# Kernel tuning notes

Measured on AMD Instinct MI355X. Metric: run time of the kernel, lower is better.

The kernel has to match this reference:

```python
import jax, jax.numpy as jnp
import numpy as np

N, E, F, H, L = 10000, 200000, 28, 256, 6
NUM_ATOM, NUM_BOND = 100, 24

def ssp(x):
    # shifted softplus used by SchNet
    return jax.nn.softplus(x) - jnp.log(2.0)

def setup_inputs() -> dict:
    key = jax.random.key(0)
    ks = iter(jax.random.split(key, 64))
    def nrm(shape, scale=0.05):
        return jax.random.normal(next(ks), shape, dtype=jnp.float32) * scale
    inp = {}
    inp['atom_type'] = jax.random.randint(next(ks), (N,), 0, NUM_ATOM)
    inp['r_feat'] = jax.random.normal(next(ks), (N, F), dtype=jnp.float32)
    inp['p_feat'] = jax.random.normal(next(ks), (N, F), dtype=jnp.float32)
    inp['pos'] = jax.random.normal(next(ks), (N, 3), dtype=jnp.float32) * 3.0
    inp['edge_index'] = jax.random.randint(next(ks), (2, E), 0, N)
    inp['edge_type_r'] = jax.random.randint(next(ks), (E,), 0, NUM_BOND)
    inp['edge_type_p'] = jax.random.randint(next(ks), (E,), 0, NUM_BOND)
    # learned parameters
    inp['atom_emb_table'] = nrm((NUM_ATOM, H // 2), 1.0)
    inp['feat_W'] = nrm((F, H // 2))                       # atom_feat_embedding (no bias)
    inp['bond_emb_table'] = nrm((NUM_BOND, H), 1.0)        # edge encoder bond embedding
    inp['edge_mlp_W1'] = nrm((1, H)); inp['edge_mlp_b1'] = jnp.zeros((H,), jnp.float32)
    inp['edge_mlp_W2'] = nrm((H, H)); inp['edge_mlp_b2'] = jnp.zeros((H,), jnp.float32)
    inp['cat_W1'] = nrm((2 * H, H)); inp['cat_b1'] = jnp.zeros((H,), jnp.float32)
    inp['cat_W2'] = nrm((H, H)); inp['cat_b2'] = jnp.zeros((H,), jnp.float32)
    # SchNet interaction blocks, stacked over L layers
    inp['filt_W1'] = nrm((L, H, H)); inp['filt_b1'] = jnp.zeros((L, H), jnp.float32)
    inp['filt_W2'] = nrm((L, H, H)); inp['filt_b2'] = jnp.zeros((L, H), jnp.float32)
    inp['lin1_W'] = nrm((L, H, H))
    inp['lin2_W'] = nrm((L, H, H)); inp['lin2_b'] = jnp.zeros((L, H), jnp.float32)
    inp['lin3_W'] = nrm((L, H, H)); inp['lin3_b'] = jnp.zeros((L, H), jnp.float32)
    # grad_global_dist_mlp: 2H -> H -> H/2 -> 1
    inp['grad_W1'] = nrm((2 * H, H)); inp['grad_b1'] = jnp.zeros((H,), jnp.float32)
    inp['grad_W2'] = nrm((H, H // 2)); inp['grad_b2'] = jnp.zeros((H // 2,), jnp.float32)
    inp['grad_W3'] = nrm((H // 2, 1)); inp['grad_b3'] = jnp.zeros((1,), jnp.float32)
    return inp

def _forward(r_feat, p_feat, pos, atom_emb_table, feat_W, bond_emb_table,
             edge_mlp_W1, edge_mlp_b1, edge_mlp_W2, edge_mlp_b2,
             cat_W1, cat_b1, cat_W2, cat_b2,
             filt_W1, filt_b1, filt_W2, filt_b2,
             lin1_W, lin2_W, lin2_b, lin3_W, lin3_b,
             grad_W1, grad_b1, grad_W2, grad_b2, grad_W3, grad_b3,
             atom_type, edge_index, edge_type_r, edge_type_p):
    src, dst = edge_index[0], edge_index[1]
    # node embedding: z = [atom_emb + feat(r), feat(p) - feat(r)]
    ar = r_feat @ feat_W
    ap = p_feat @ feat_W
    z = jnp.concatenate([atom_emb_table[atom_type] + ar, ap - ar], axis=-1)  # (N, H)
    # edge lengths (E, 1)
    d = pos[src] - pos[dst]
    edge_length = jnp.sqrt(jnp.sum(d * d, axis=-1, keepdims=True) + 1e-12)
    # condensed edge embedding 'bond_w_d': mlp(d) * bond_emb(type), r/p branches, then edge_cat MLP
    d_emb = ssp(edge_length @ edge_mlp_W1 + edge_mlp_b1) @ edge_mlp_W2 + edge_mlp_b2  # (E, H)
    attr_r = d_emb * bond_emb_table[edge_type_r]
    attr_p = d_emb * bond_emb_table[edge_type_p]
    edge_attr = jax.nn.relu(jnp.concatenate([attr_r, attr_p], -1) @ cat_W1 + cat_b1) @ cat_W2 + cat_b2  # (E, H)
    # SchNet encoder: L CFConv interaction blocks with residual
    nn_ = z.shape[0]
    def layer(h, p):
        fW1, fb1, fW2, fb2, l1, l2, l2b, l3, l3b = p
        Wf = ssp(edge_attr @ fW1 + fb1) @ fW2 + fb2            # (E, H) continuous filters
        msg = (h @ l1)[src] * Wf                               # gather + modulate
        agg = jax.ops.segment_sum(msg, dst, num_segments=nn_)  # scatter-add to nodes
        return h + (ssp(agg @ l2 + l2b) @ l3 + l3b), None
    node_attr, _ = jax.lax.scan(layer, z, (filt_W1, filt_b1, filt_W2, filt_b2, lin1_W, lin2_W, lin2_b, lin3_W, lin3_b))
    # assemble_atom_pair_feature: [h_row * h_col, edge_attr] -> (E, 2H)
    h_pair = jnp.concatenate([node_attr[src] * node_attr[dst], edge_attr], axis=-1)
    h = jax.nn.relu(h_pair @ grad_W1 + grad_b1)
    h = jax.nn.relu(h @ grad_W2 + grad_b2)
    edge_inv = h @ grad_W3 + grad_b3                           # (E, 1)
    return edge_inv, edge_length

def reference(atom_type, r_feat, p_feat, pos, edge_index, edge_type_r, edge_type_p,
              atom_emb_table, feat_W, bond_emb_table,
              edge_mlp_W1, edge_mlp_b1, edge_mlp_W2, edge_mlp_b2,
              cat_W1, cat_b1, cat_W2, cat_b2,
              filt_W1, filt_b1, filt_W2, filt_b2,
              lin1_W, lin2_W, lin2_b, lin3_W, lin3_b,
              grad_W1, grad_b1, grad_W2, grad_b2, grad_W3, grad_b3):
    return _forward(r_feat, p_feat, pos, atom_emb_table, feat_W, bond_emb_table,
                    edge_mlp_W1, edge_mlp_b1, edge_mlp_W2, edge_mlp_b2,
                    cat_W1, cat_b1, cat_W2, cat_b2,
                    filt_W1, filt_b1, filt_W2, filt_b2,
                    lin1_W, lin2_W, lin2_b, lin3_W, lin3_b,
                    grad_W1, grad_b1, grad_W2, grad_b2, grad_W3, grad_b3,
                    atom_type, edge_index, edge_type_r, edge_type_p)
```

## Files before the change

kernel.cpp:

```cpp
#include <hip/hip_runtime.h>
#include <hip/hip_bf16.h>
#include <math.h>

#define HDIM 256

typedef unsigned short u16;
typedef short short8 __attribute__((ext_vector_type(8)));
typedef _Float16 f16x8 __attribute__((ext_vector_type(8)));
typedef float f32x4 __attribute__((ext_vector_type(4)));

__device__ __forceinline__ float sspf(float x) {
  const float LOG2E = 1.4426950408889634f, LN2 = 0.6931471805599453f;
  float t = exp2f(-fabsf(x) * LOG2E);
  return fmaxf(x, 0.f) + (log2f(1.f + t) - 1.f) * LN2;
}
__device__ __forceinline__ float bf2f(u16 u) {
  union { unsigned int i; float f; } x; x.i = ((unsigned int)u) << 16; return x.f;
}
__device__ __forceinline__ u16 f2bf(float f) {
  union { float f; unsigned int i; } x; x.f = f;
  unsigned int r = x.i + 0x7FFFu + ((x.i >> 16) & 1u);
  return (u16)(r >> 16);
}
__device__ __forceinline__ u16 f2h_bits(float f) {
  _Float16 h = (_Float16)f;
  return __builtin_bit_cast(unsigned short, h);
}
__device__ __forceinline__ float4 ld4f(const float* p) { return *(const float4*)p; }

__device__ __forceinline__ int iw_idx(int row, int col) {
  return row * 256 + ((((col >> 3) ^ (row & 7)) << 3) | (col & 7));
}
__device__ __forceinline__ int ir_idx(int row, int cchunk) {
  return row * 256 + ((cchunk ^ (row & 7)) << 3);
}

template<int DT>
__device__ __forceinline__ f32x4 mma(short8 a, short8 b, f32x4 c) {
  if constexpr (DT == 0)
    return __builtin_amdgcn_mfma_f32_16x16x32_bf16(a, b, c, 0, 0, 0);
  else
    return __builtin_amdgcn_mfma_f32_16x16x32_f16(__builtin_bit_cast(f16x8, a),
                                                  __builtin_bit_cast(f16x8, b), c, 0, 0, 0);
}

__device__ __forceinline__ void zacc(f32x4 (&acc)[4][4]) {
#pragma unroll
  for (int i = 0; i < 4; ++i)
#pragma unroll
    for (int j = 0; j < 4; ++j) { acc[i][j][0]=0.f; acc[i][j][1]=0.f; acc[i][j][2]=0.f; acc[i][j][3]=0.f; }
}

template<int NSTEPS, int BT_N, int NTW, int DT, bool WRAP8, typename ATR>
__device__ __forceinline__ void gemm44(f32x4 (&acc)[4][4], const u16* __restrict__ bt,
                                       const u16* __restrict__ inter,
                                       int w, int m, int quad, ATR atr) {
  short8 bf[2][NTW];
#pragma unroll
  for (int nt = 0; nt < NTW; ++nt)
    bf[0][nt] = *(const short8*)(bt + (w * (NTW * 16) + nt * 16 + m) * 32 + quad * 8);
#pragma unroll
  for (int ks = 0; ks < NSTEPS; ++ks) {
    const int cur = ks & 1, nxt = cur ^ 1;
    if (ks + 1 < NSTEPS) {
#pragma unroll
      for (int nt = 0; nt < NTW; ++nt)
        bf[nxt][nt] = *(const short8*)(bt + (size_t)(ks + 1) * (BT_N * 32)
                                       + (w * (NTW * 16) + nt * 16 + m) * 32 + quad * 8);
    }
    int kchunk = (WRAP8 ? (ks & 7) : ks) * 4 + quad;
#pragma unroll
    for (int mt = 0; mt < 4; ++mt) {
      short8 af = *(const short8*)&inter[ir_idx(mt * 16 + m, kchunk)];
      af = atr(mt, ks, af);
#pragma unroll
      for (int nt = 0; nt < NTW; ++nt)
        acc[mt][nt] = mma<DT>(af, bf[cur][nt], acc[mt][nt]);
    }
  }
}

template<int NTW, int ACT, int OF>
__device__ __forceinline__ void store_inter44(u16* inter, int w, int m, int quad,
                                              const f32x4 (&acc)[4][4], const float* bias) {
#pragma unroll
  for (int mt = 0; mt < 4; ++mt)
#pragma unroll
    for (int nt = 0; nt < NTW; ++nt) {
      int col = w * (NTW * 16) + nt * 16 + m;
      float bv = bias[col];
#pragma unroll
      for (int r = 0; r < 4; ++r) {
        int row = mt * 16 + quad * 4 + r;
        float x = acc[mt][nt][r] + bv;
        if (ACT == 1) x = fmaxf(x, 0.f);
        else if (ACT == 2) x = sspf(x);
        inter[iw_idx(row, col)] = (OF == 0) ? f2bf(x) : f2h_bits(x);
      }
    }
}

__device__ __forceinline__ void copy_out_nt(u16* C, int row0, const u16* inter, int t) {
#pragma unroll
  for (int c = 0; c < 8; ++c) {
    int idx = c * 256 + t;
    int row = idx >> 5, c8 = idx & 31;
    int src = (c8 ^ (row & 7)) << 3;
    short8 v = *(const short8*)&inter[row * 256 + src];
    __builtin_nontemporal_store(v, (short8*)(C + (size_t)(row0 + row) * HDIM + c8 * 8));
  }
}

template<int NTW, int ACT, int CM>
__device__ __forceinline__ void store_node44(float* C, int row0, int w, int m, int quad,
                                             const f32x4 (&acc)[4][4], const float* bias, int M) {
#pragma unroll
  for (int mt = 0; mt < 4; ++mt)
#pragma unroll
    for (int nt = 0; nt < NTW; ++nt) {
      int col = w * (NTW * 16) + nt * 16 + m;
      float bv = bias ? bias[col] : 0.f;
#pragma unroll
      for (int r = 0; r < 4; ++r) {
        int row = row0 + mt * 16 + quad * 4 + r;
        if (row < M) {
          float x = acc[mt][nt][r] + bv;
          if (ACT == 2) x = sspf(x);
          size_t idx = (size_t)row * HDIM + col;
          if (CM == 1) x += C[idx];
          C[idx] = x;
        }
      }
    }
}

struct EncArgs {
  const int* se_e; const float* lenp; const float* W1; const float* b1;
  const u16* btA; const float* bA;
  const float* bondT; const int* etr; const int* etp;
  const u16* btB; const float* bB;
  const u16* btC; const float* bC;
  u16* outp;
};
__global__ __launch_bounds__(256, 3) void encoder_k(EncArgs a) {
  __shared__ u16 inter[64 * 256];
  __shared__ u16 bondL[24 * 264];
  const int t = threadIdx.x;
  const int w = t >> 6, lane = t & 63, m = lane & 15, quad = lane >> 4;
  const int row0 = blockIdx.x * 64;
  auto idt = [](int, int, short8 v) { return v; };

  for (int i = t; i < 24 * 256; i += 256) {
    int r = i >> 8, c = i & 255;
    bondL[r * 264 + c] = f2h_bits(a.bondT[r * 256 + c]);
  }
  int brv[4], bpv[4];
#pragma unroll
  for (int mt = 0; mt < 4; ++mt) {
    int eo = a.se_e[row0 + mt * 16 + m];
    brv[mt] = a.etr[eo]; bpv[mt] = a.etp[eo];
  }
  {
    int row = t >> 2;
    float len = a.lenp[a.se_e[row0 + row]];
#pragma unroll
    for (int c = 0; c < 8; ++c) {
      int chunk = (t & 3) + c * 4, k = chunk * 8;
      float4 w0 = ld4f(a.W1 + k), w1 = ld4f(a.W1 + k + 4);
      float4 c0 = ld4f(a.b1 + k), c1 = ld4f(a.b1 + k + 4);
      short8 v;
      v[0] = (short)f2bf(sspf(len * w0.x + c0.x)); v[1] = (short)f2bf(sspf(len * w0.y + c0.y));
      v[2] = (short)f2bf(sspf(len * w0.z + c0.z)); v[3] = (short)f2bf(sspf(len * w0.w + c0.w));
      v[4] = (short)f2bf(sspf(len * w1.x + c1.x)); v[5] = (short)f2bf(sspf(len * w1.y + c1.y));
      v[6] = (short)f2bf(sspf(len * w1.z + c1.z)); v[7] = (short)f2bf(sspf(len * w1.w + c1.w));
      *(short8*)&inter[row * 256 + ((chunk ^ (row & 7)) << 3)] = v;
    }
  }
  __syncthreads();
  f32x4 acc[4][4];
  zacc(acc);
  gemm44<8, 256, 4, 0, false>(acc, a.btA, inter, w, m, quad, idt);
  __syncthreads();
  store_inter44<4, 0, 1>(inter, w, m, quad, acc, a.bA);
  __syncthreads();
  zacc(acc);
  auto atrB = [&](int mt, int ks, short8 v) -> short8 {
    int k2 = (ks & 7) * 32 + quad * 8;
    int et = (ks < 8) ? brv[mt] : bpv[mt];
    f16x8 dv = __builtin_bit_cast(f16x8, v);
    f16x8 bd = __builtin_bit_cast(f16x8, *(const short8*)&bondL[et * 264 + k2]);
    return __builtin_bit_cast(short8, dv * bd);
  };
  gemm44<16, 256, 4, 1, true>(acc, a.btB, inter, w, m, quad, atrB);
  __syncthreads();
  store_inter44<4, 1, 0>(inter, w, m, quad, acc, a.bB);
  __syncthreads();
  zacc(acc);
  gemm44<8, 256, 4, 0, false>(acc, a.btC, inter, w, m, quad, idt);
  __syncthreads();
  store_inter44<4, 0, 0>(inter, w, m, quad, acc, a.bC);
  __syncthreads();
  copy_out_nt(a.outp, row0, inter, t);
}

struct FiltArgs { const u16* inA; const u16* bt1; const float* b1; const u16* bt2; const float* b2; u16* outp; };
__global__ __launch_bounds__(256, 3) void filt_k(FiltArgs a) {
  __shared__ u16 inter[64 * 256];
  const int t = threadIdx.x;
  const int w = t >> 6, lane = t & 63, m = lane & 15, quad = lane >> 4;
  const int row0 = blockIdx.x * 64;
  auto idt = [](int, int, short8 v) { return v; };
  {
    int row = t >> 2;
#pragma unroll
    for (int c = 0; c < 8; ++c) {
      int chunk = (t & 3) + c * 4;
      short8 v = __builtin_nontemporal_load((const short8*)(a.inA + (size_t)(row0 + row) * HDIM + chunk * 8));
      *(short8*)&inter[row * 256 + ((chunk ^ (row & 7)) << 3)] = v;
    }
  }
  __syncthreads();
  f32x4 acc[4][4];
  zacc(acc);
  gemm44<8, 256, 4, 0, false>(acc, a.bt1, inter, w, m, quad, idt);
  __syncthreads();
  store_inter44<4, 2, 0>(inter, w, m, quad, acc, a.b1);
  __syncthreads();
  zacc(acc);
  gemm44<8, 256, 4, 0, false>(acc, a.bt2, inter, w, m, quad, idt);
  __syncthreads();
  store_inter44<4, 0, 0>(inter, w, m, quad, acc, a.b2);
  __syncthreads();
  copy_out_nt(a.outp, row0, inter, t);
}

struct GradArgs {
  const float* h; const int* se_src; const int* se_dst; const int* se_e;
  const u16* eA; const u16* bt1; const float* b1; const u16* bt2; const float* b2;
  const float* W3; const float* b3; float* outp;
};
__global__ __launch_bounds__(256, 3) void gradf_k(GradArgs a) {
  __shared__ u16 inter[64 * 256];
  const int t = threadIdx.x;
  const int w = t >> 6, lane = t & 63, m = lane & 15, quad = lane >> 4;
  const int row0 = blockIdx.x * 64;
  auto idt = [](int, int, short8 v) { return v; };
  {
    int row = t >> 2;
    int s = a.se_src[row0 + row], d = a.se_dst[row0 + row];
#pragma unroll
    for (int c = 0; c < 8; ++c) {
      int chunk = (t & 3) + c * 4, k = chunk * 8;
      const float* xp = a.h + (size_t)s * HDIM + k;
      const float* yp = a.h + (size_t)d * HDIM + k;
      float4 x0 = ld4f(xp), x1 = ld4f(xp + 4);
      float4 y0 = ld4f(yp), y1 = ld4f(yp + 4);
      short8 v;
      v[0] = (short)f2bf(x0.x * y0.x); v[1] = (short)f2bf(x0.y * y0.y);
      v[2] = (short)f2bf(x0.z * y0.z); v[3] = (short)f2bf(x0.w * y0.w);
      v[4] = (short)f2bf(x1.x * y1.x); v[5] = (short)f2bf(x1.y * y1.y);
      v[6] = (short)f2bf(x1.z * y1.z); v[7] = (short)f2bf(x1.w * y1.w);
      *(short8*)&inter[row * 256 + ((chunk ^ (row & 7)) << 3)] = v;
    }
  }
  __syncthreads();
  f32x4 acc[4][4];
  zacc(acc);
  gemm44<8, 256, 4, 0, false>(acc, a.bt1, inter, w, m, quad, idt);
  __syncthreads();
  {
    int row = t >> 2;
#pragma unroll
    for (int c = 0; c < 8; ++c) {
      int chunk = (t & 3) + c * 4;
      short8 v = __builtin_nontemporal_load((const short8*)(a.eA + (size_t)(row0 + row) * HDIM + chunk * 8));
      *(short8*)&inter[row * 256 + ((chunk ^ (row & 7)) << 3)] = v;
    }
  }
  __syncthreads();
  gemm44<8, 256, 4, 0, false>(acc, a.bt1 + 8 * 256 * 32, inter, w, m, quad, idt);
  __syncthreads();
  store_inter44<4, 1, 0>(inter, w, m, quad, acc, a.b1);
  __syncthreads();
  zacc(acc);
  gemm44<8, 128, 2, 0, false>(acc, a.bt2, inter, w, m, quad, idt);
  float p[4][4];
#pragma unroll
  for (int mt = 0; mt < 4; ++mt) { p[mt][0]=0.f; p[mt][1]=0.f; p[mt][2]=0.f; p[mt][3]=0.f; }
#pragma unroll
  for (int mt = 0; mt < 4; ++mt)
#pragma unroll
    for (int nt = 0; nt < 2; ++nt) {
      int col = w * 32 + nt * 16 + m;
      float w3 = a.W3[col], bv = a.b2[col];
#pragma unroll
      for (int r = 0; r < 4; ++r) p[mt][r] += fmaxf(acc[mt][nt][r] + bv, 0.f) * w3;
    }
  __syncthreads();
  float* red = (float*)inter;
#pragma unroll
  for (int mt = 0; mt < 4; ++mt)
#pragma unroll
    for (int r = 0; r < 4; ++r)
      red[(mt * 16 + quad * 4 + r) * 68 + w * 16 + m] = p[mt][r];
  __syncthreads();
  if (t < 64) {
    float s = a.b3[0];
#pragma unroll
    for (int i = 0; i < 64; ++i) s += red[t * 68 + i];
    a.outp[a.se_e[row0 + t]] = s;
  }
}

struct LinArgs { const float* A; const u16* bt; float* C; int M; };
__global__ __launch_bounds__(256, 3) void lin1_k(LinArgs a) {
  __shared__ u16 inter[64 * 256];
  const int t = threadIdx.x;
  const int w = t >> 6, lane = t & 63, m = lane & 15, quad = lane >> 4;
  const int row0 = blockIdx.x * 64;
  auto idt = [](int, int, short8 v) { return v; };
  {
    int row = t >> 2, grow = row0 + row;
#pragma unroll
    for (int c = 0; c < 8; ++c) {
      int chunk = (t & 3) + c * 4, k = chunk * 8;
      short8 v;
      if (grow < a.M) {
        const float* p = a.A + (size_t)grow * HDIM + k;
        float4 x0 = ld4f(p), x1 = ld4f(p + 4);
        v[0]=(short)f2bf(x0.x); v[1]=(short)f2bf(x0.y); v[2]=(short)f2bf(x0.z); v[3]=(short)f2bf(x0.w);
        v[4]=(short)f2bf(x1.x); v[5]=(short)f2bf(x1.y); v[6]=(short)f2bf(x1.z); v[7]=(short)f2bf(x1.w);
      } else { v = short8{0,0,0,0,0,0,0,0}; }
      *(short8*)&inter[row * 256 + ((chunk ^ (row & 7)) << 3)] = v;
    }
  }
  __syncthreads();
  f32x4 acc[4][4];
  zacc(acc);
  gemm44<8, 256, 4, 0, false>(acc, a.bt, inter, w, m, quad, idt);
  store_node44<4, 0, 0>(a.C, row0, w, m, quad, acc, nullptr, a.M);
}

struct Lin23Args { const float* A; const u16* bt2; const float* b2; const u16* bt3; const float* b3; float* C; int M; };
__global__ __launch_bounds__(256, 3) void lin23_k(Lin23Args a) {
  __shared__ u16 inter[64 * 256];
  const int t = threadIdx.x;
  const int w = t >> 6, lane = t & 63, m = lane & 15, quad = lane >> 4;
  const int row0 = blockIdx.x * 64;
  auto idt = [](int, int, short8 v) { return v; };
  {
    int row = t >> 2, grow = row0 + row;
#pragma unroll
    for (int c = 0; c < 8; ++c) {
      int chunk = (t & 3) + c * 4, k = chunk * 8;
      short8 v;
      if (grow < a.M) {
        const float* p = a.A + (size_t)grow * HDIM + k;
        float4 x0 = ld4f(p), x1 = ld4f(p + 4);
        v[0]=(short)f2bf(x0.x); v[1]=(short)f2bf(x0.y); v[2]=(short)f2bf(x0.z); v[3]=(short)f2bf(x0.w);
        v[4]=(short)f2bf(x1.x); v[5]=(short)f2bf(x1.y); v[6]=(short)f2bf(x1.z); v[7]=(short)f2bf(x1.w);
      } else { v = short8{0,0,0,0,0,0,0,0}; }
      *(short8*)&inter[row * 256 + ((chunk ^ (row & 7)) << 3)] = v;
    }
  }
  __syncthreads();
  f32x4 acc[4][4];
  zacc(acc);
  gemm44<8, 256, 4, 0, false>(acc, a.bt2, inter, w, m, quad, idt);
  __syncthreads();
  store_inter44<4, 2, 0>(inter, w, m, quad, acc, a.b2);
  __syncthreads();
  zacc(acc);
  gemm44<8, 256, 4, 0, false>(acc, a.bt3, inter, w, m, quad, idt);
  store_node44<4, 0, 1>(a.C, row0, w, m, quad, acc, a.b3, a.M);
}

struct WTDesc { const float* src; u16* dst; int K; int Nshift; int fmt; };
struct WTList { WTDesc d[35]; };
__global__ __launch_bounds__(256) void wtrans_k(WTList wl) {
  WTDesc e = wl.d[blockIdx.y];
  int total = e.K << e.Nshift;
  int idx = blockIdx.x * 256 + threadIdx.x;
  if (idx >= total) return;
  int k = idx >> e.Nshift;
  int n = idx & ((1 << e.Nshift) - 1);
  float v = e.src[idx];
  e.dst[((size_t)(k >> 5) << (e.Nshift + 5)) + n * 32 + (k & 31)] = e.fmt ? f2h_bits(v) : f2bf(v);
}

__global__ void node_embed_k(const int* atom_type, const float* r_feat, const float* p_feat,
                             const float* emb, const float* fW, float* z, int N, int F) {
  int n = blockIdx.x;
  int j = threadIdx.x;
  __shared__ float rr[32], pp[32];
  if (j < F) { rr[j] = r_feat[(size_t)n * F + j]; pp[j] = p_feat[(size_t)n * F + j]; }
  __syncthreads();
  float ar = 0.f, ap = 0.f;
  for (int f = 0; f < F; ++f) {
    float wv = fW[f * 128 + j];
    ar += rr[f] * wv;
    ap += pp[f] * wv;
  }
  int at = atom_type[n];
  z[(size_t)n * HDIM + j] = emb[at * 128 + j] + ar;
  z[(size_t)n * HDIM + 128 + j] = ap - ar;
}

__global__ void edge_geom_k(const float* pos, const int* src, const int* dst, float* len_out, int E) {
  int e = blockIdx.x * blockDim.x + threadIdx.x;
  if (e >= E) return;
  int s = src[e], d = dst[e];
  float dx = pos[s * 3 + 0] - pos[d * 3 + 0];
  float dy = pos[s * 3 + 1] - pos[d * 3 + 1];
  float dz = pos[s * 3 + 2] - pos[d * 3 + 2];
  len_out[e] = sqrtf(dx * dx + dy * dy + dz * dz + 1e-12f);
}

__global__ void zero_k(float4* p, int n4) {
  int i = blockIdx.x * 256 + threadIdx.x;
  if (i < n4) p[i] = make_float4(0.f, 0.f, 0.f, 0.f);
}
__global__ void zero_int_k(int* p, int n) {
  int i = blockIdx.x * 256 + threadIdx.x;
  if (i < n) p[i] = 0;
}
__global__ void hist_k(const int* dst, int* cnt, int E) {
  int e = blockIdx.x * 256 + threadIdx.x;
  if (e < E) atomicAdd(&cnt[dst[e]], 1);
}
__global__ __launch_bounds__(256) void scan_k(const int* cnt, int* rowstart, int N) {
  __shared__ int part[256];
  int t = threadIdx.x;
  int chunk = (N + 255) / 256;
  int lo = t * chunk, hi = lo + chunk; if (hi > N) hi = N; if (lo > N) lo = N;
  int s = 0;
  for (int i = lo; i < hi; ++i) s += cnt[i];
  part[t] = s;
  __syncthreads();
  for (int off = 1; off < 256; off <<= 1) {
    int v = (t >= off) ? part[t - off] : 0;
    __syncthreads();
    part[t] += v;
    __syncthreads();
  }
  int run = (t == 0) ? 0 : part[t - 1];
  for (int i = lo; i < hi; ++i) { rowstart[i] = run; run += cnt[i]; }
  if (t == 255) rowstart[N] = run;
}
__global__ void fill_k(const int* src, const int* dst, const int* rowstart, int* cursor,
                       int* se_src, int* se_dst, int* se_e, int E) {
  int e = blockIdx.x * 256 + threadIdx.x;
  if (e >= E) return;
  int d = dst[e];
  int p = atomicAdd(&cursor[d], 1);
  int idx = rowstart[d] + p;
  se_src[idx] = src[e];
  se_dst[idx] = d;
  se_e[idx] = e;
}

__global__ __launch_bounds__(256) void gather_k(const float* hh, const u16* Wf,
                                                const int* se_src, const int* rowstart,
                                                float* agg, int N) {
  int n = blockIdx.x;
  int j = threadIdx.x;
  int s0 = rowstart[n], s1 = rowstart[n + 1];
  float acc = 0.f;
  for (int i = s0; i < s1; ++i) {
    u16 wv = __builtin_nontemporal_load(Wf + (size_t)i * HDIM + j);
    acc += hh[(size_t)se_src[i] * HDIM + j] * bf2f(wv);
  }
  agg[(size_t)n * HDIM + j] = acc;
}

extern "C" void kernel_launch(void* const* d_in, const int* in_sizes, int n_in,
                              void* d_out, int out_size, void* d_ws, size_t ws_size,
                              hipStream_t stream) {
  const int* atom_type = (const int*)d_in[0];
  const float* r_feat  = (const float*)d_in[1];
  const float* p_feat  = (const float*)d_in[2];
  const float* pos     = (const float*)d_in[3];
  const int* eidx      = (const int*)d_in[4];
  const int* etype_r   = (const int*)d_in[5];
  const int* etype_p   = (const int*)d_in[6];
  const float* atom_emb = (const float*)d_in[7];
  const float* feat_W   = (const float*)d_in[8];
  const float* bondT    = (const float*)d_in[9];
  const float* e_W1     = (const float*)d_in[10];
  const float* e_b1     = (const float*)d_in[11];
  const float* e_W2     = (const float*)d_in[12];
  const float* e_b2     = (const float*)d_in[13];
  const float* cat_W1   = (const float*)d_in[14];
  const float* cat_b1   = (const float*)d_in[15];
  const float* cat_W2   = (const float*)d_in[16];
  const float* cat_b2   = (const float*)d_in[17];
  const float* filt_W1  = (const float*)d_in[18];
  const float* filt_b1  = (const float*)d_in[19];
  const float* filt_W2  = (const float*)d_in[20];
  const float* filt_b2  = (const float*)d_in[21];
  const float* lin1_W   = (const float*)d_in[22];
  const float* lin2_W   = (const float*)d_in[23];
  const float* lin2_b   = (const float*)d_in[24];
  const float* lin3_W   = (const float*)d_in[25];
  const float* lin3_b   = (const float*)d_in[26];
  const float* grad_W1  = (const float*)d_in[27];
  const float* grad_b1  = (const float*)d_in[28];
  const float* grad_W2  = (const float*)d_in[29];
  const float* grad_b2  = (const float*)d_in[30];
  const float* grad_W3  = (const float*)d_in[31];
  const float* grad_b3  = (const float*)d_in[32];

  const int N = in_sizes[0];
  const int F = in_sizes[1] / N;
  const int E = in_sizes[4] / 2;
  const int L = in_sizes[18] / (HDIM * HDIM);
  const int* srcI = eidx;
  const int* dstI = eidx + E;
  float* out = (float*)d_out;

  const size_t BT_ELEMS = (size_t)(32 * 65536 + 2 * 131072 + 32768);
  size_t need = 2 * (size_t)E * HDIM * 2 + 3 * (size_t)N * HDIM * 4 + BT_ELEMS * 2
              + (size_t)(3 * E + 3 * N + 1) * 4 + 64;
  if (ws_size < need) {
    int n4 = (out_size + 3) / 4;
    zero_k<<<(n4 + 255) / 256, 256, 0, stream>>>((float4*)d_out, n4);
    return;
  }
  char* base = (char*)d_ws;
  u16* eA = (u16*)base; base += (size_t)E * HDIM * 2;
  u16* Wf = (u16*)base; base += (size_t)E * HDIM * 2;
  float* h   = (float*)base; base += (size_t)N * HDIM * 4;
  float* hh  = (float*)base; base += (size_t)N * HDIM * 4;
  float* agg = (float*)base; base += (size_t)N * HDIM * 4;
  u16* bt = (u16*)base; base += BT_ELEMS * 2;
  int* se_src = (int*)base; base += (size_t)E * 4;
  int* se_dst = (int*)base; base += (size_t)E * 4;
  int* se_e   = (int*)base; base += (size_t)E * 4;
  int* cnt    = (int*)base; base += (size_t)N * 4;
  int* cursor = (int*)base; base += (size_t)N * 4;
  int* rowstart = (int*)base; base += ((size_t)N + 1) * 4;

  size_t off = 0;
  u16* bt_eW2  = bt + off; off += 65536;
  u16* bt_cat1 = bt + off; off += 131072;
  u16* bt_cat2 = bt + off; off += 65536;
  u16* bt_f1[6]; u16* bt_f2[6]; u16* bt_l1[6]; u16* bt_l2[6]; u16* bt_l3[6];
  for (int l = 0; l < 6; ++l) { bt_f1[l] = bt + off; off += 65536; }
  for (int l = 0; l < 6; ++l) { bt_f2[l] = bt + off; off += 65536; }
  for (int l = 0; l < 6; ++l) { bt_l1[l] = bt + off; off += 65536; }
  for (int l = 0; l < 6; ++l) { bt_l2[l] = bt + off; off += 65536; }
  for (int l = 0; l < 6; ++l) { bt_l3[l] = bt + off; off += 65536; }
  u16* bt_g1 = bt + off; off += 131072;
  u16* bt_g2 = bt + off; off += 32768;

  WTList wl;
  int wi = 0;
  wl.d[wi++] = WTDesc{e_W2, bt_eW2, 256, 8, 0};
  wl.d[wi++] = WTDesc{cat_W1, bt_cat1, 512, 8, 1};
  wl.d[wi++] = WTDesc{cat_W2, bt_cat2, 256, 8, 0};
  for (int l = 0; l < 6; ++l) wl.d[wi++] = WTDesc{filt_W1 + (size_t)l * 65536, bt_f1[l], 256, 8, 0};
  for (int l = 0; l < 6; ++l) wl.d[wi++] = WTDesc{filt_W2 + (size_t)l * 65536, bt_f2[l], 256, 8, 0};
  for (int l = 0; l < 6; ++l) wl.d[wi++] = WTDesc{lin1_W + (size_t)l * 65536, bt_l1[l], 256, 8, 0};
  for (int l = 0; l < 6; ++l) wl.d[wi++] = WTDesc{lin2_W + (size_t)l * 65536, bt_l2[l], 256, 8, 0};
  for (int l = 0; l < 6; ++l) wl.d[wi++] = WTDesc{lin3_W + (size_t)l * 65536, bt_l3[l], 256, 8, 0};
  wl.d[wi++] = WTDesc{grad_W1, bt_g1, 512, 8, 0};
  wl.d[wi++] = WTDesc{grad_W2, bt_g2, 256, 7, 0};
  wtrans_k<<<dim3(512, 35), 256, 0, stream>>>(wl);

  const int EB = E / 64;
  const int NBK = (N + 63) / 64;
  const int EBLK = (E + 255) / 256;

  zero_int_k<<<(2 * N + 255) / 256, 256, 0, stream>>>(cnt, 2 * N);
  hist_k<<<EBLK, 256, 0, stream>>>(dstI, cnt, E);
  scan_k<<<1, 256, 0, stream>>>(cnt, rowstart, N);
  fill_k<<<EBLK, 256, 0, stream>>>(srcI, dstI, rowstart, cursor, se_src, se_dst, se_e, E);

  node_embed_k<<<N, 128, 0, stream>>>(atom_type, r_feat, p_feat, atom_emb, feat_W, h, N, F);
  edge_geom_k<<<EBLK, 256, 0, stream>>>(pos, srcI, dstI, out + E, E);

  EncArgs ea;
  ea.se_e = se_e; ea.lenp = out + E; ea.W1 = e_W1; ea.b1 = e_b1;
  ea.btA = bt_eW2; ea.bA = e_b2;
  ea.bondT = bondT; ea.etr = etype_r; ea.etp = etype_p;
  ea.btB = bt_cat1; ea.bB = cat_b1;
  ea.btC = bt_cat2; ea.bC = cat_b2;
  ea.outp = eA;
  encoder_k<<<EB, 256, 0, stream>>>(ea);

  for (int l = 0; l < L; ++l) {
    const size_t bo = (size_t)l * HDIM;
    FiltArgs fa{eA, bt_f1[l], filt_b1 + bo, bt_f2[l], filt_b2 + bo, Wf};
    filt_k<<<EB, 256, 0, stream>>>(fa);
    LinArgs la{h, bt_l1[l], hh, N};
    lin1_k<<<NBK, 256, 0, stream>>>(la);
    gather_k<<<N, 256, 0, stream>>>(hh, Wf, se_src, rowstart, agg, N);
    Lin23Args l23{agg, bt_l2[l], lin2_b + bo, bt_l3[l], lin3_b + bo, h, N};
    lin23_k<<<NBK, 256, 0, stream>>>(l23);
  }

  GradArgs ga;
  ga.h = h; ga.se_src = se_src; ga.se_dst = se_dst; ga.se_e = se_e;
  ga.eA = eA; ga.bt1 = bt_g1; ga.b1 = grad_b1; ga.bt2 = bt_g2; ga.b2 = grad_b2;
  ga.W3 = grad_W3; ga.b3 = grad_b3; ga.outp = out;
  gradf_k<<<EB, 256, 0, stream>>>(ga);
}
```

Measured before the change: 1.790 ms.

## Merge filter MLP and lin1 into one launch; drop nontemporal hints

Combines the per-layer filter-network kernel and the lin1 node GEMM into a single grid whose blocks branch on block index, so the small lin1 work shares the launch with the edge GEMMs. This removes one launch per layer and the tail idle time between the two kernels. Separately, all nontemporal loads and stores on eA/Wf are replaced with ordinary accesses so the Wf written by the filter kernel can stay in cache for the gather kernel. The trade-off is more cache pollution and a heterogeneous grid.

```diff
diff --git a/kernel.cpp b/kernel.cpp
--- a/kernel.cpp
+++ b/kernel.cpp
@@ -100,14 +100,13 @@
     }
 }
 
-__device__ __forceinline__ void copy_out_nt(u16* C, int row0, const u16* inter, int t) {
+__device__ __forceinline__ void copy_out(u16* C, int row0, const u16* inter, int t) {
 #pragma unroll
   for (int c = 0; c < 8; ++c) {
     int idx = c * 256 + t;
     int row = idx >> 5, c8 = idx & 31;
     int src = (c8 ^ (row & 7)) << 3;
-    short8 v = *(const short8*)&inter[row * 256 + src];
-    __builtin_nontemporal_store(v, (short8*)(C + (size_t)(row0 + row) * HDIM + c8 * 8));
+    *(short8*)(C + (size_t)(row0 + row) * HDIM + c8 * 8) = *(const short8*)&inter[row * 256 + src];
   }
 }
 
@@ -200,38 +199,66 @@
   __syncthreads();
   store_inter44<4, 0, 0>(inter, w, m, quad, acc, a.bC);
   __syncthreads();
-  copy_out_nt(a.outp, row0, inter, t);
-}
-
-struct FiltArgs { const u16* inA; const u16* bt1; const float* b1; const u16* bt2; const float* b2; u16* outp; };
-__global__ __launch_bounds__(256, 3) void filt_k(FiltArgs a) {
+  copy_out(a.outp, row0, inter, t);
+}
+
+struct FL1Args {
+  const u16* eA; const u16* bt1; const float* b1; const u16* bt2; const float* b2; u16* Wf;
+  int EBlocks;
+  const float* h; const u16* btL; float* hh; int M;
+};
+__global__ __launch_bounds__(256, 3) void fl1_k(FL1Args a) {
   __shared__ u16 inter[64 * 256];
   const int t = threadIdx.x;
   const int w = t >> 6, lane = t & 63, m = lane & 15, quad = lane >> 4;
-  const int row0 = blockIdx.x * 64;
   auto idt = [](int, int, short8 v) { return v; };
-  {
-    int row = t >> 2;
-#pragma unroll
-    for (int c = 0; c < 8; ++c) {
-      int chunk = (t & 3) + c * 4;
-      short8 v = __builtin_nontemporal_load((const short8*)(a.inA + (size_t)(row0 + row) * HDIM + chunk * 8));
-      *(short8*)&inter[row * 256 + ((chunk ^ (row & 7)) << 3)] = v;
-    }
-  }
-  __syncthreads();
-  f32x4 acc[4][4];
-  zacc(acc);
-  gemm44<8, 256, 4, 0, false>(acc, a.bt1, inter, w, m, quad, idt);
-  __syncthreads();
-  store_inter44<4, 2, 0>(inter, w, m, quad, acc, a.b1);
-  __syncthreads();
-  zacc(acc);
-  gemm44<8, 256, 4, 0, false>(acc, a.bt2, inter, w, m, quad, idt);
-  __syncthreads();
-  store_inter44<4, 0, 0>(inter, w, m, quad, acc, a.b2);
-  __syncthreads();
-  copy_out_nt(a.outp, row0, inter, t);
+  if ((int)blockIdx.x < a.EBlocks) {
+    const int row0 = blockIdx.x * 64;
+    {
+      int row = t >> 2;
+#pragma unroll
+      for (int c = 0; c < 8; ++c) {
+        int chunk = (t & 3) + c * 4;
+        short8 v = *(const short8*)(a.eA + (size_t)(row0 + row) * HDIM + chunk * 8);
+        *(short8*)&inter[row * 256 + ((chunk ^ (row & 7)) << 3)] = v;
+      }
+    }
+    __syncthreads();
+    f32x4 acc[4][4];
+    zacc(acc);
+    gemm44<8, 256, 4, 0, false>(acc, a.bt1, inter, w, m, quad, idt);
+    __syncthreads();
+    store_inter44<4, 2, 0>(inter, w, m, quad, acc, a.b1);
+    __syncthreads();
+    zacc(acc);
+    gemm44<8, 256, 4, 0, false>(acc, a.bt2, inter, w, m, quad, idt);
+    __syncthreads();
+    store_inter44<4, 0, 0>(inter, w, m, quad, acc, a.b2);
+    __syncthreads();
+    copy_out(a.Wf, row0, inter, t);
+  } else {
+    const int row0 = ((int)blockIdx.x - a.EBlocks) * 64;
+    {
+      int row = t >> 2, grow = row0 + row;
+#pragma unroll
+      for (int c = 0; c < 8; ++c) {
+        int chunk = (t & 3) + c * 4, k = chunk * 8;
+        short8 v;
+        if (grow < a.M) {
+          const float* p = a.h + (size_t)grow * HDIM + k;
+          float4 x0 = ld4f(p), x1 = ld4f(p + 4);
+          v[0]=(short)f2bf(x0.x); v[1]=(short)f2bf(x0.y); v[2]=(short)f2bf(x0.z); v[3]=(short)f2bf(x0.w);
+          v[4]=(short)f2bf(x1.x); v[5]=(short)f2bf(x1.y); v[6]=(short)f2bf(x1.z); v[7]=(short)f2bf(x1.w);
+        } else { v = short8{0,0,0,0,0,0,0,0}; }
+        *(short8*)&inter[row * 256 + ((chunk ^ (row & 7)) << 3)] = v;
+      }
+    }
+    __syncthreads();
+    f32x4 acc[4][4];
+    zacc(acc);
+    gemm44<8, 256, 4, 0, false>(acc, a.btL, inter, w, m, quad, idt);
+    store_node44<4, 0, 0>(a.hh, row0, w, m, quad, acc, nullptr, a.M);
+  }
 }
 
 struct GradArgs {
@@ -273,7 +300,7 @@
 #pragma unroll
     for (int c = 0; c < 8; ++c) {
       int chunk = (t & 3) + c * 4;
-      short8 v = __builtin_nontemporal_load((const short8*)(a.eA + (size_t)(row0 + row) * HDIM + chunk * 8));
+      short8 v = *(const short8*)(a.eA + (size_t)(row0 + row) * HDIM + chunk * 8);
       *(short8*)&inter[row * 256 + ((chunk ^ (row & 7)) << 3)] = v;
     }
   }
@@ -310,35 +337,6 @@
     for (int i = 0; i < 64; ++i) s += red[t * 68 + i];
     a.outp[a.se_e[row0 + t]] = s;
   }
-}
-
-struct LinArgs { const float* A; const u16* bt; float* C; int M; };
-__global__ __launch_bounds__(256, 3) void lin1_k(LinArgs a) {
-  __shared__ u16 inter[64 * 256];
-  const int t = threadIdx.x;
-  const int w = t >> 6, lane = t & 63, m = lane & 15, quad = lane >> 4;
-  const int row0 = blockIdx.x * 64;
-  auto idt = [](int, int, short8 v) { return v; };
-  {
-    int row = t >> 2, grow = row0 + row;
-#pragma unroll
-    for (int c = 0; c < 8; ++c) {
-      int chunk = (t & 3) + c * 4, k = chunk * 8;
-      short8 v;
-      if (grow < a.M) {
-        const float* p = a.A + (size_t)grow * HDIM + k;
-        float4 x0 = ld4f(p), x1 = ld4f(p + 4);
-        v[0]=(short)f2bf(x0.x); v[1]=(short)f2bf(x0.y); v[2]=(short)f2bf(x0.z); v[3]=(short)f2bf(x0.w);
-        v[4]=(short)f2bf(x1.x); v[5]=(short)f2bf(x1.y); v[6]=(short)f2bf(x1.z); v[7]=(short)f2bf(x1.w);
-      } else { v = short8{0,0,0,0,0,0,0,0}; }
-      *(short8*)&inter[row * 256 + ((chunk ^ (row & 7)) << 3)] = v;
-    }
-  }
-  __syncthreads();
-  f32x4 acc[4][4];
-  zacc(acc);
-  gemm44<8, 256, 4, 0, false>(acc, a.bt, inter, w, m, quad, idt);
-  store_node44<4, 0, 0>(a.C, row0, w, m, quad, acc, nullptr, a.M);
 }
 
 struct Lin23Args { const float* A; const u16* bt2; const float* b2; const u16* bt3; const float* b3; float* C; int M; };
@@ -466,10 +464,8 @@
   int j = threadIdx.x;
   int s0 = rowstart[n], s1 = rowstart[n + 1];
   float acc = 0.f;
-  for (int i = s0; i < s1; ++i) {
-    u16 wv = __builtin_nontemporal_load(Wf + (size_t)i * HDIM + j);
-    acc += hh[(size_t)se_src[i] * HDIM + j] * bf2f(wv);
-  }
+  for (int i = s0; i < s1; ++i)
+    acc += hh[(size_t)se_src[i] * HDIM + j] * bf2f(Wf[(size_t)i * HDIM + j]);
   agg[(size_t)n * HDIM + j] = acc;
 }
 
@@ -590,10 +586,11 @@
 
   for (int l = 0; l < L; ++l) {
     const size_t bo = (size_t)l * HDIM;
-    FiltArgs fa{eA, bt_f1[l], filt_b1 + bo, bt_f2[l], filt_b2 + bo, Wf};
-    filt_k<<<EB, 256, 0, stream>>>(fa);
-    LinArgs la{h, bt_l1[l], hh, N};
-    lin1_k<<<NBK, 256, 0, stream>>>(la);
+    FL1Args fl;
+    fl.eA = eA; fl.bt1 = bt_f1[l]; fl.b1 = filt_b1 + bo; fl.bt2 = bt_f2[l]; fl.b2 = filt_b2 + bo;
+    fl.Wf = Wf; fl.EBlocks = EB;
+    fl.h = h; fl.btL = bt_l1[l]; fl.hh = hh; fl.M = N;
+    fl1_k<<<EB + NBK, 256, 0, stream>>>(fl);
     gather_k<<<N, 256, 0, stream>>>(hh, Wf, se_src, rowstart, agg, N);
     Lin23Args l23{agg, bt_l2[l], lin2_b + bo, bt_l3[l], lin3_b + bo, h, N};
     lin23_k<<<NBK, 256, 0, stream>>>(l23);
```

Measured after the change: 1.614 ms. -9.8%, faster.
